# Performance work log

Measured on AMD Instinct MI355X. Metric: run time of the kernel, lower is better.

The kernel has to match this reference:

```python
import jax, jax.numpy as jnp
import numpy as np

STRIDE = 1
PADDING = 1

def setup_inputs() -> dict:
    key = jax.random.key(0)
    k1, k2 = jax.random.split(key)
    x = jax.random.normal(k1, (32, 128, 56, 56), dtype=jnp.float32)
    # kaiming_uniform_(a=sqrt(5)) -> U(-bound, bound), bound = sqrt(6/((1+5)*fan_in)) = 1/sqrt(fan_in)
    fan_in = 128 * 3 * 3
    bound = 1.0 / np.sqrt(fan_in)
    weight = jax.random.uniform(k2, (256, 128, 3, 3), dtype=jnp.float32, minval=-bound, maxval=bound)
    bias = jnp.zeros((256,), dtype=jnp.float32)
    return {"x": x, "weight": weight, "bias": bias}

def reference(x, weight, bias):
    # Dense 2D convolution (cross-correlation, matching torch semantics), NCHW/OIHW.
    out = jax.lax.conv_general_dilated(
        x, weight,
        window_strides=(STRIDE, STRIDE),
        padding=[(PADDING, PADDING), (PADDING, PADDING)],
        dimension_numbers=("NCHW", "OIHW", "NCHW"),
    )
    return out + bias[None, :, None, None]
```

## Files before the change

### kernel.cpp

```cpp
#include <hip/hip_runtime.h>

typedef __bf16 bfvec8 __attribute__((ext_vector_type(8)));
typedef float f32x4 __attribute__((ext_vector_type(4)));
typedef unsigned short u16x8 __attribute__((ext_vector_type(8)));
typedef unsigned int u32;

constexpr int C_IN = 128, Wd = 56, Hd = 56, HW = 3136, K_OUT = 256, N_IMG = 32;
constexpr int KKTOT = 1152;
constexpr int WP = 58;
constexpr size_t XP_ELEMS = (size_t)N_IMG * WP * WP * C_IN;
constexpr size_t XP_BYTES = XP_ELEMS * 2;
constexpr size_t WT_ELEMS = (size_t)9 * 4 * 2 * 128 * 32;
constexpr size_t WS_NEED  = XP_BYTES + WT_ELEMS * 2;

__device__ inline unsigned short f2bf(float f) {
    union { float f; unsigned u; } v; v.f = f;
    unsigned u = v.u;
    u += 0x7fffu + ((u >> 16) & 1u);
    return (unsigned short)(u >> 16);
}

__device__ inline void gld16(const void* g, void* l) {
    __builtin_amdgcn_global_load_lds(
        (const __attribute__((address_space(1))) u32*)g,
        (__attribute__((address_space(3))) u32*)l, 16, 0, 0);
}

#define CFENCE() asm volatile("" ::: "memory")

__global__ __launch_bounds__(256) void xpose(const float* __restrict__ x,
                                             unsigned short* __restrict__ xp) {
    __shared__ unsigned short T[Wd * C_IN];
    const int nb = blockIdx.x;
    const int n = nb / Hd, h = nb - n * Hd;
    const float* src = x + (size_t)n * C_IN * HW + h * Wd;
    #pragma unroll
    for (int k = 0; k < 7; ++k) {
        int idx = threadIdx.x + k * 256;
        int c = idx / 14, w4 = idx - c * 14;
        const float4 v = *(const float4*)(src + (size_t)c * HW + w4 * 4);
        const int sw = (w4 & 15) * 8;
        T[(w4 * 4 + 0) * C_IN + (c ^ sw)] = f2bf(v.x);
        T[(w4 * 4 + 1) * C_IN + (c ^ sw)] = f2bf(v.y);
        T[(w4 * 4 + 2) * C_IN + (c ^ sw)] = f2bf(v.z);
        T[(w4 * 4 + 3) * C_IN + (c ^ sw)] = f2bf(v.w);
    }
    __syncthreads();
    unsigned short* dst = xp + ((size_t)(n * WP + h + 1) * WP + 1) * C_IN;
    const u16x8* s8 = (const u16x8*)T;
    u16x8* d8 = (u16x8*)dst;
    #pragma unroll
    for (int k = 0; k < 4; ++k) {
        int idx = threadIdx.x + k * 256;
        if (idx < 896) {
            int w = idx >> 4, j8 = idx & 15;
            d8[idx] = s8[w * 16 + (j8 ^ ((w >> 2) & 15))];
        }
    }
}

__global__ __launch_bounds__(256) void wxform(const float* __restrict__ w,
                                              unsigned short* __restrict__ wt) {
    int o = blockIdx.x * 256 + threadIdx.x;
    int kk = o & 31, n = (o >> 5) & 127, nt = (o >> 12) & 1,
        ch = (o >> 13) & 3, rs = o >> 15;
    float v = w[(size_t)(nt * 128 + n) * KKTOT + (ch * 32 + kk) * 9 + rs];
    wt[o] = f2bf(v);
}

__global__ __launch_bounds__(256) void conv_gemm(
    const unsigned short* __restrict__ xp, const unsigned short* __restrict__ wt,
    const float* __restrict__ bias, float* __restrict__ out)
{
    __shared__ __align__(16) unsigned short As[3][128 * 32];
    __shared__ __align__(16) unsigned short Bs[3][128 * 32];

    const int tid = threadIdx.x;
    const int hbx = blockIdx.x;
    const int lbx = (hbx & 7) * 196 + (hbx >> 3);
    const int nt  = lbx & 1;
    const int mtile = (lbx >> 1) * 128;

    const int cg8 = ((tid & 3) ^ ((tid >> 3) & 3)) * 8;

    const unsigned short *gA0, *gA1;
    {
        int mrow = tid >> 2;
        int m = mtile + mrow;
        int ni = m / HW; int hw = m - ni * HW; int h = hw / Wd; int w = hw - h * Wd;
        gA0 = xp + ((size_t)(ni * WP + h + 1) * WP + (w + 1)) * C_IN + cg8;
        m += 64;
        ni = m / HW; hw = m - ni * HW; h = hw / Wd; w = hw - h * Wd;
        gA1 = xp + ((size_t)(ni * WP + h + 1) * WP + (w + 1)) * C_IN + cg8;
    }
    const unsigned short* gB = wt + (size_t)nt * 4096 + (size_t)(tid & 0xFC) * 8 + cg8;

    const int wave = tid >> 6, lane = tid & 63;
    const int wrow = (wave >> 1) * 64, wcol = (wave & 1) * 64;
    const int r16 = lane & 15, quad = lane >> 4;
    const int qsw = (quad ^ ((r16 >> 1) & 3)) * 8;

    const f32x4 zero4 = {0.f, 0.f, 0.f, 0.f};
    f32x4 acc[4][4];
    #pragma unroll
    for (int i = 0; i < 4; ++i)
        #pragma unroll
        for (int j = 0; j < 4; ++j)
            acc[i][j] = zero4;

    auto issue = [&](int step, int buf) {
        const int rs = step >> 2, ch = step & 3;
        const int dr = rs / 3 - 1, dc = rs % 3 - 1;
        const int aoff = (dr * WP + dc) * C_IN + ch * 32;
        const size_t boff = (size_t)step * 8192;
        gld16(gA0 + aoff, (void*)(As[buf] + tid * 8));
        gld16(gA1 + aoff, (void*)(As[buf] + 2048 + tid * 8));
        gld16(gB + boff,        (void*)(Bs[buf] + tid * 8));
        gld16(gB + boff + 2048, (void*)(Bs[buf] + 2048 + tid * 8));
    };

    issue(0, 0);
    issue(1, 1);

    #pragma unroll
    for (int step = 0; step < 36; ++step) {
        const int cur = step % 3;

        CFENCE(); __builtin_amdgcn_s_barrier(); CFENCE();
        if (step < 34) {
            issue(step + 2, (step + 2) % 3);
            asm volatile("s_waitcnt vmcnt(8)" ::: "memory");
        } else if (step == 34) {
            asm volatile("s_waitcnt vmcnt(4)" ::: "memory");
        } else {
            asm volatile("s_waitcnt vmcnt(0)" ::: "memory");
        }
        CFENCE(); __builtin_amdgcn_s_barrier(); CFENCE();

        bfvec8 af[4], bf[4];
        #pragma unroll
        for (int mi = 0; mi < 4; ++mi)
            af[mi] = *(const bfvec8*)&As[cur][(wrow + mi * 16 + r16) * 32 + qsw];
        #pragma unroll
        for (int ni = 0; ni < 4; ++ni)
            bf[ni] = *(const bfvec8*)&Bs[cur][(wcol + ni * 16 + r16) * 32 + qsw];

        #pragma unroll
        for (int mi = 0; mi < 4; ++mi)
            #pragma unroll
            for (int ni = 0; ni < 4; ++ni)
                acc[mi][ni] = __builtin_amdgcn_mfma_f32_16x16x32_bf16(
                    af[mi], bf[ni], acc[mi][ni], 0, 0, 0);
    }

    const int ntile = nt * 128;
    #pragma unroll
    for (int ni = 0; ni < 4; ++ni) {
        const int k = ntile + wcol + ni * 16 + r16;
        const float bb = bias[k];
        #pragma unroll
        for (int mi = 0; mi < 4; ++mi) {
            const int mb  = mtile + wrow + mi * 16 + quad * 4;
            const int ne  = mb / HW;
            const int hwe = mb - ne * HW;
            f32x4 v;
            #pragma unroll
            for (int i = 0; i < 4; ++i) v[i] = acc[mi][ni][i] + bb;
            *(f32x4*)(out + ((size_t)ne * K_OUT + k) * HW + hwe) = v;
        }
    }
}

extern "C" void kernel_launch(void* const* d_in, const int* in_sizes, int n_in,
                              void* d_out, int out_size, void* d_ws, size_t ws_size,
                              hipStream_t stream) {
    const float* x    = (const float*)d_in[0];
    const float* wgt  = (const float*)d_in[1];
    const float* bias = (const float*)d_in[2];
    float* out = (float*)d_out;

    unsigned short* xp = (unsigned short*)d_ws;
    unsigned short* wt = (unsigned short*)((char*)d_ws + XP_BYTES);

    hipMemsetAsync(d_ws, 0, XP_BYTES, stream);
    xpose<<<dim3(N_IMG * Hd), dim3(256), 0, stream>>>(x, xp);
    wxform<<<dim3((int)(WT_ELEMS / 256)), dim3(256), 0, stream>>>(wgt, wt);
    conv_gemm<<<dim3(1568), dim3(256), 0, stream>>>(xp, wt, bias, out);
}
```

Measured before the change: 215.1 us.

## Fuse prep kernels, zero only halo, load weights straight to registers

The memset, transpose and weight-transform launches become one prep kernel. That kernel zeroes only the padding halo of the padded input instead of clearing the whole buffer. In the GEMM, weight fragments are now loaded from global memory directly into double-buffered registers rather than staged through LDS. This halves shared-memory use, which may raise occupancy, and removes the B-side LDS reads. The trade-off is more per-lane global loads that depend on L2 hits, plus extra register pressure from holding B fragments.

```diff
diff --git a/kernel.cpp b/kernel.cpp
--- a/kernel.cpp
+++ b/kernel.cpp
@@ -11,7 +11,11 @@
 constexpr size_t XP_ELEMS = (size_t)N_IMG * WP * WP * C_IN;
 constexpr size_t XP_BYTES = XP_ELEMS * 2;
 constexpr size_t WT_ELEMS = (size_t)9 * 4 * 2 * 128 * 32;
-constexpr size_t WS_NEED  = XP_BYTES + WT_ELEMS * 2;
+
+constexpr int HALO_BLKS = 456;
+constexpr int WT_BLKS   = 1152;
+constexpr int XPOSE_BLKS = N_IMG * Hd;
+constexpr int PREP_GRID = HALO_BLKS + WT_BLKS + XPOSE_BLKS;
 
 __device__ inline unsigned short f2bf(float f) {
     union { float f; unsigned u; } v; v.f = f;
@@ -28,10 +32,35 @@
 
 #define CFENCE() asm volatile("" ::: "memory")
 
-__global__ __launch_bounds__(256) void xpose(const float* __restrict__ x,
-                                             unsigned short* __restrict__ xp) {
+__global__ __launch_bounds__(256) void prep(const float* __restrict__ x,
+                                            const float* __restrict__ wgt,
+                                            unsigned short* __restrict__ xp,
+                                            unsigned short* __restrict__ wt) {
     __shared__ unsigned short T[Wd * C_IN];
-    const int nb = blockIdx.x;
+    const int bx = blockIdx.x;
+
+    if (bx < HALO_BLKS) {
+        int v = bx * 256 + threadIdx.x;
+        int n = v / 3648, rem = v - n * 3648;
+        int p = rem >> 4, c8 = rem & 15;
+        int hh, ww;
+        if (p < 58)       { hh = 0;       ww = p;       }
+        else if (p < 116) { hh = 57;      ww = p - 58;  }
+        else if (p < 172) { hh = p - 115; ww = 0;       }
+        else              { hh = p - 171; ww = 57;      }
+        const u16x8 z = {0, 0, 0, 0, 0, 0, 0, 0};
+        *(u16x8*)(xp + ((size_t)(n * WP + hh) * WP + ww) * C_IN + c8 * 8) = z;
+        return;
+    }
+    if (bx < HALO_BLKS + WT_BLKS) {
+        int o = (bx - HALO_BLKS) * 256 + threadIdx.x;
+        int kk = o & 31, n = (o >> 5) & 127, nt = (o >> 12) & 1,
+            ch = (o >> 13) & 3, rs = o >> 15;
+        float v = wgt[(size_t)(nt * 128 + n) * KKTOT + (ch * 32 + kk) * 9 + rs];
+        wt[o] = f2bf(v);
+        return;
+    }
+    const int nb = bx - (HALO_BLKS + WT_BLKS);
     const int n = nb / Hd, h = nb - n * Hd;
     const float* src = x + (size_t)n * C_IN * HW + h * Wd;
     #pragma unroll
@@ -59,21 +88,11 @@
     }
 }
 
-__global__ __launch_bounds__(256) void wxform(const float* __restrict__ w,
-                                              unsigned short* __restrict__ wt) {
-    int o = blockIdx.x * 256 + threadIdx.x;
-    int kk = o & 31, n = (o >> 5) & 127, nt = (o >> 12) & 1,
-        ch = (o >> 13) & 3, rs = o >> 15;
-    float v = w[(size_t)(nt * 128 + n) * KKTOT + (ch * 32 + kk) * 9 + rs];
-    wt[o] = f2bf(v);
-}
-
 __global__ __launch_bounds__(256) void conv_gemm(
     const unsigned short* __restrict__ xp, const unsigned short* __restrict__ wt,
     const float* __restrict__ bias, float* __restrict__ out)
 {
     __shared__ __align__(16) unsigned short As[3][128 * 32];
-    __shared__ __align__(16) unsigned short Bs[3][128 * 32];
 
     const int tid = threadIdx.x;
     const int hbx = blockIdx.x;
@@ -93,13 +112,14 @@
         ni = m / HW; hw = m - ni * HW; h = hw / Wd; w = hw - h * Wd;
         gA1 = xp + ((size_t)(ni * WP + h + 1) * WP + (w + 1)) * C_IN + cg8;
     }
-    const unsigned short* gB = wt + (size_t)nt * 4096 + (size_t)(tid & 0xFC) * 8 + cg8;
 
     const int wave = tid >> 6, lane = tid & 63;
     const int wrow = (wave >> 1) * 64, wcol = (wave & 1) * 64;
     const int r16 = lane & 15, quad = lane >> 4;
     const int qsw = (quad ^ ((r16 >> 1) & 3)) * 8;
 
+    const unsigned short* gBf = wt + (size_t)nt * 4096 + (wcol + r16) * 32 + quad * 8;
+
     const f32x4 zero4 = {0.f, 0.f, 0.f, 0.f};
     f32x4 acc[4][4];
     #pragma unroll
@@ -108,27 +128,34 @@
         for (int j = 0; j < 4; ++j)
             acc[i][j] = zero4;
 
-    auto issue = [&](int step, int buf) {
+    bfvec8 bf[2][4];
+
+    auto issueA = [&](int step, int buf) {
         const int rs = step >> 2, ch = step & 3;
         const int dr = rs / 3 - 1, dc = rs % 3 - 1;
         const int aoff = (dr * WP + dc) * C_IN + ch * 32;
-        const size_t boff = (size_t)step * 8192;
         gld16(gA0 + aoff, (void*)(As[buf] + tid * 8));
         gld16(gA1 + aoff, (void*)(As[buf] + 2048 + tid * 8));
-        gld16(gB + boff,        (void*)(Bs[buf] + tid * 8));
-        gld16(gB + boff + 2048, (void*)(Bs[buf] + 2048 + tid * 8));
     };
-
-    issue(0, 0);
-    issue(1, 1);
+    auto loadB = [&](int step, int par) {
+        #pragma unroll
+        for (int ni = 0; ni < 4; ++ni)
+            bf[par][ni] = *(const bfvec8*)(gBf + (size_t)step * 8192 + ni * 512);
+    };
+
+    issueA(0, 0);
+    loadB(0, 0);
+    issueA(1, 1);
 
     #pragma unroll
     for (int step = 0; step < 36; ++step) {
         const int cur = step % 3;
+        const int par = step & 1;
 
         CFENCE(); __builtin_amdgcn_s_barrier(); CFENCE();
+        if (step < 35) loadB(step + 1, par ^ 1);
+        if (step < 34) issueA(step + 2, (step + 2) % 3);
         if (step < 34) {
-            issue(step + 2, (step + 2) % 3);
             asm volatile("s_waitcnt vmcnt(8)" ::: "memory");
         } else if (step == 34) {
             asm volatile("s_waitcnt vmcnt(4)" ::: "memory");
@@ -137,20 +164,17 @@
         }
         CFENCE(); __builtin_amdgcn_s_barrier(); CFENCE();
 
-        bfvec8 af[4], bf[4];
+        bfvec8 af[4];
         #pragma unroll
         for (int mi = 0; mi < 4; ++mi)
             af[mi] = *(const bfvec8*)&As[cur][(wrow + mi * 16 + r16) * 32 + qsw];
-        #pragma unroll
-        for (int ni = 0; ni < 4; ++ni)
-            bf[ni] = *(const bfvec8*)&Bs[cur][(wcol + ni * 16 + r16) * 32 + qsw];
 
         #pragma unroll
         for (int mi = 0; mi < 4; ++mi)
             #pragma unroll
             for (int ni = 0; ni < 4; ++ni)
                 acc[mi][ni] = __builtin_amdgcn_mfma_f32_16x16x32_bf16(
-                    af[mi], bf[ni], acc[mi][ni], 0, 0, 0);
+                    af[mi], bf[par][ni], acc[mi][ni], 0, 0, 0);
     }
 
     const int ntile = nt * 128;
@@ -182,8 +206,6 @@
     unsigned short* xp = (unsigned short*)d_ws;
     unsigned short* wt = (unsigned short*)((char*)d_ws + XP_BYTES);
 
-    hipMemsetAsync(d_ws, 0, XP_BYTES, stream);
-    xpose<<<dim3(N_IMG * Hd), dim3(256), 0, stream>>>(x, xp);
-    wxform<<<dim3((int)(WT_ELEMS / 256)), dim3(256), 0, stream>>>(wgt, wt);
+    prep<<<dim3(PREP_GRID), dim3(256), 0, stream>>>(x, wgt, xp, wt);
     conv_gemm<<<dim3(1568), dim3(256), 0, stream>>>(xp, wt, bias, out);
 }
```

Result: slower. 225.4 us (+4.8%).
